# Kernel tuning notes

Hardware: AMD Instinct MI355X
Metric: run time of the kernel (lower is better)

The kernel has to match this reference:

```python
import jax, jax.numpy as jnp
import numpy as np

SX, SY, C, K = 256, 256, 3, 15
DD, DT, SIGMA = 5, 0.2, 0.65
C0 = tuple(i % C for i in range(K))
C1 = tuple(tuple(i for i in range(K) if i % C == c) for c in range(C))
MA = DD - SIGMA  # flow magnitude bound


def _sobel(A):
    # A: (X, Y, c) -> (X, Y, 2, c); matches jsp.signal.convolve2d(..., mode='same')
    kx = jnp.array([[1., 0., -1.], [2., 0., -2.], [1., 0., -1.]], dtype=A.dtype)
    ky = kx.T
    # convolve2d flips the kernel; emulate true convolution by correlating with rot180 kernels
    kern = jnp.stack([jnp.rot90(ky, 2), jnp.rot90(kx, 2)])[:, None]  # (2,1,3,3): [grad_y, grad_x]
    x = jnp.transpose(A, (2, 0, 1))[:, None]                          # (c,1,X,Y)
    out = jax.lax.conv_general_dilated(x, kern, (1, 1), 'SAME')       # (c,2,X,Y)
    return jnp.transpose(out, (2, 3, 1, 0))                           # (X,Y,2,c)


def _reintegration(A, P, F):
    # Reintegration tracking, has_hidden=True, border='wall', mix='softmax'
    xs, ys = jnp.meshgrid(jnp.arange(SX), jnp.arange(SY))
    pos = (jnp.dstack((ys, xs)) + .5).astype(A.dtype)     # (X,Y,2) cell centers (row, col)
    mus = pos[..., None] + jnp.clip(DT * F, -MA, MA)      # (X,Y,2,C) target centers
    mus = jnp.clip(mus, SIGMA, SX - SIGMA)                # wall border
    shifts = jnp.array([(dx, dy) for dx in range(-DD, DD + 1) for dy in range(-DD, DD + 1)])
    cap = min(1., 2 * SIGMA)

    def step(sft):
        sh = (sft[0], sft[1])
        Ar = jnp.roll(A, sh, axis=(0, 1))
        Pr = jnp.roll(P, sh, axis=(0, 1))
        mur = jnp.roll(mus, sh, axis=(0, 1))
        dpmu = jnp.abs(pos[..., None] - mur)              # (X,Y,2,C)
        sz = .5 - dpmu + SIGMA
        area = jnp.prod(jnp.clip(sz, 0., cap), axis=2) / (4 * SIGMA ** 2)  # (X,Y,C)
        return Ar * area, Pr

    nA, nP = jax.vmap(step)(shifts)                       # (N,X,Y,C), (N,X,Y,K)
    expnA = jnp.exp(nA.sum(-1, keepdims=True)) - 1.       # softmax mix rule
    newA = nA.sum(0)
    newP = (nP * expnA).sum(0) / (expnA.sum(0) + 1e-10)
    return newA, newP


def _forward(A, P, fK_real, fK_imag, m, s):
    fK = fK_real + 1j * fK_imag                           # (X,Y,K) kernel FFTs
    fA = jnp.fft.fft2(A, axes=(0, 1))                     # (X,Y,C)
    fAk = jnp.take(fA, jnp.array(C0), axis=2)             # (X,Y,K) per-kernel source channel
    U = jnp.real(jnp.fft.ifft2(fK * fAk, axes=(0, 1)))    # (X,Y,K)
    U = (2. * jnp.exp(-((U - m) ** 2) / (2. * s ** 2)) - 1.) * P  # growth(U,m,s)*P
    U = jnp.dstack([U[:, :, C1[c]].sum(-1) for c in range(C)])    # (X,Y,C)
    F = _sobel(U)                                         # (X,Y,2,C)
    Cg = _sobel(A.sum(-1, keepdims=True))                 # (X,Y,2,1)
    alpha = jnp.clip((A[:, :, None, :] / 2.) ** 2, 0., 1.)
    F = jnp.clip(F * (1. - alpha) - Cg * alpha, -MA, MA)
    return _reintegration(A, P, F)


def setup_inputs() -> dict:
    key = jax.random.key(0)
    kA, kP, kr, km, ks, ka, kb, kw = jax.random.split(key, 8)
    A = jax.random.uniform(kA, (SX, SY, C), dtype=jnp.float32)
    P = jax.random.uniform(kP, (SX, SY, K), dtype=jnp.float32)
    R = 15.0
    r = jax.random.uniform(kr, (K,), minval=.2, maxval=1.)
    m = jax.random.uniform(km, (K,), minval=.05, maxval=.5, dtype=jnp.float32)
    s = jax.random.uniform(ks, (K,), minval=.001, maxval=.18, dtype=jnp.float32)
    a = jax.random.uniform(ka, (K, 3))
    b = jax.random.uniform(kb, (K, 3), minval=.001, maxval=1.)
    w = jax.random.uniform(kw, (K, 3), minval=.01, maxval=.5)
    mid = SX // 2
    D = jnp.linalg.norm(jnp.mgrid[-mid:mid, -mid:mid], axis=0)[..., None] / ((R + 15.) * r)  # (X,Y,K)
    Kk = jax.nn.sigmoid(-(D - 1.) * 10.) * (b * jnp.exp(-((D[..., None] - a) / w) ** 2)).sum(-1)
    nK = Kk / Kk.sum((0, 1), keepdims=True)
    fK = jnp.fft.fft2(jnp.fft.fftshift(nK, axes=(0, 1)), axes=(0, 1))
    return {"A": A, "P": P,
            "fK_real": jnp.real(fK).astype(jnp.float32),
            "fK_imag": jnp.imag(fK).astype(jnp.float32),
            "m": m, "s": s}


def reference(A, P, fK_real, fK_imag, m, s):
    return _forward(A, P, fK_real, fK_imag, m, s)
```

## Files before the change

### kernel.cpp

```cpp
#include <hip/hip_runtime.h>


#define XY  65536
#define NC  3
#define NK  15
#define WPAD 260

__device__ __forceinline__ float2 cmul(float2 a, float2 b) {
  return make_float2(a.x * b.x - a.y * b.y, a.x * b.y + a.y * b.x);
}

__device__ __forceinline__ void fft256_lds(float2* b0, float2* b1, int t, float sign) {
  float2* src = b0;
  float2* dst = b1;
#pragma unroll
  for (int stage = 0; stage < 4; ++stage) {
    __syncthreads();
    const int Ns = 1 << (2 * stage);
    float2 v0 = src[t];
    float2 v1 = src[t + 64];
    float2 v2 = src[t + 128];
    float2 v3 = src[t + 192];
    const int jm = t & (Ns - 1);
    float ang = sign * 6.283185307179586f * (float)jm / (float)(Ns * 4);
    float sn, cs;
    __sincosf(ang, &sn, &cs);
    float2 w1 = make_float2(cs, sn);
    float2 w2 = cmul(w1, w1);
    float2 w3 = cmul(w2, w1);
    v1 = cmul(v1, w1);
    v2 = cmul(v2, w2);
    v3 = cmul(v3, w3);
    float2 a0 = make_float2(v0.x + v2.x, v0.y + v2.y);
    float2 a1 = make_float2(v0.x - v2.x, v0.y - v2.y);
    float2 a2 = make_float2(v1.x + v3.x, v1.y + v3.y);
    float2 a3 = make_float2(v1.x - v3.x, v1.y - v3.y);
    float2 ia3 = make_float2(-sign * a3.y, sign * a3.x);
    const int idxD = ((t >> (2 * stage)) << (2 * stage)) * 4 + jm;
    dst[idxD]          = make_float2(a0.x + a2.x, a0.y + a2.y);
    dst[idxD + Ns]     = make_float2(a1.x + ia3.x, a1.y + ia3.y);
    dst[idxD + 2 * Ns] = make_float2(a0.x - a2.x, a0.y - a2.y);
    dst[idxD + 3 * Ns] = make_float2(a1.x - ia3.x, a1.y - ia3.y);
    float2* tmp = src; src = dst; dst = tmp;
  }
  __syncthreads();
}

__global__ __launch_bounds__(256) void k_prep(const float* __restrict__ A,
                                              const float* __restrict__ P,
                                              float* __restrict__ Aplan,
                                              float* __restrict__ Asum,
                                              float* __restrict__ Pplan) {
  const int b = blockIdx.x * 256 + threadIdx.x;
  float a0 = A[b * 3 + 0], a1 = A[b * 3 + 1], a2 = A[b * 3 + 2];
  Aplan[0 * XY + b] = a0;
  Aplan[1 * XY + b] = a1;
  Aplan[2 * XY + b] = a2;
  Asum[b] = a0 + a1 + a2;
#pragma unroll
  for (int k = 0; k < NK; ++k) Pplan[k * XY + b] = P[b * NK + k];
}

__global__ __launch_bounds__(256) void k_rowfft(const float* __restrict__ Aplan,
                                                float2* __restrict__ RF) {
  __shared__ float2 lds0[4 * WPAD], lds1[4 * WPAD];
  const int tid = threadIdx.x;
  const int w = tid >> 6, lane = tid & 63;
  const int c = blockIdx.x >> 6;
  const int x = ((blockIdx.x & 63) << 2) + w;
  float2* b0 = lds0 + w * WPAD;
  float2* b1 = lds1 + w * WPAD;
  const float* src = Aplan + c * XY + x * 256;
#pragma unroll
  for (int r = 0; r < 4; ++r) {
    int y = lane + 64 * r;
    b0[y] = make_float2(src[y], 0.0f);
  }
  fft256_lds(b0, b1, lane, -1.0f);
#pragma unroll
  for (int r = 0; r < 4; ++r) {
    int y = lane + 64 * r;
    RF[(c * 256 + x) * 256 + y] = b0[y];
  }
}

__global__ __launch_bounds__(512, 1) void k_colfft(const float* __restrict__ fKr,
                                                   const float* __restrict__ fKi,
                                                   const float2* __restrict__ RF,
                                                   float2* __restrict__ T2) {
  __shared__ float2 lds0[8 * WPAD];
  __shared__ float2 lds1[8 * WPAD];
  const int tid = threadIdx.x;
  const int k = blockIdx.x >> 5;
  const int y0 = (blockIdx.x & 31) << 3;
  const int c = k % 3;

  {
    const int q = tid & 3;
#pragma unroll
    for (int r = 0; r < 2; ++r) {
      const int x = (tid >> 2) + (r << 7);
      const float4* src = (const float4*)(RF + (c * XY + x * 256 + y0));
      float4 v = src[q];
      lds0[(2 * q) * WPAD + x]     = make_float2(v.x, v.y);
      lds0[(2 * q + 1) * WPAD + x] = make_float2(v.z, v.w);
    }
  }

  const int w = tid >> 6, lane = tid & 63;
  float2* b0 = lds0 + w * WPAD;
  float2* b1 = lds1 + w * WPAD;
  fft256_lds(b0, b1, lane, -1.0f);

  const int y = y0 + w;
  float2 fa[4];
#pragma unroll
  for (int r = 0; r < 4; ++r) fa[r] = b0[lane + 64 * r];
#pragma unroll
  for (int r = 0; r < 4; ++r) {
    const int x = lane + 64 * r;
    const int fi = (x * 256 + y) * NK + k;
    float2 Kv = make_float2(fKr[fi], fKi[fi]);
    b0[x] = cmul(Kv, fa[r]);
  }
  fft256_lds(b0, b1, lane, 1.0f);

  {
    const int q = tid & 3;
#pragma unroll
    for (int r = 0; r < 2; ++r) {
      const int x = (tid >> 2) + (r << 7);
      float2 v0 = lds0[(2 * q) * WPAD + x];
      float2 v1 = lds0[(2 * q + 1) * WPAD + x];
      float4* dst = (float4*)(T2 + (k * XY + x * 256 + y0));
      dst[q] = make_float4(v0.x, v0.y, v1.x, v1.y);
    }
  }
}

__global__ __launch_bounds__(320, 1) void k_irowfft_growth(const float2* __restrict__ T2,
                                                           const float* __restrict__ Pplan,
                                                           const float* __restrict__ m,
                                                           const float* __restrict__ s,
                                                           float* __restrict__ Ucol) {
  __shared__ float2 lds0[5 * WPAD];
  __shared__ float2 lds1[5 * WPAD];
  __shared__ float accs[5 * WPAD];
  const int tid = threadIdx.x;
  const int x = blockIdx.x & 255;
  const int c = blockIdx.x >> 8;
  const int j = tid >> 6, lane = tid & 63;
  const int k = c + 3 * j;

  float2* b0 = lds0 + j * WPAD;
  float2* b1 = lds1 + j * WPAD;
  const float2* src = T2 + (k * XY + x * 256);
#pragma unroll
  for (int r = 0; r < 4; ++r) {
    int y = lane + 64 * r;
    b0[y] = src[y];
  }
  fft256_lds(b0, b1, lane, 1.0f);

  const float mk = m[k];
  const float sk = s[k];
  const float inv2s2 = 0.5f / (sk * sk);
  const float* pk = Pplan + k * XY + x * 256;
#pragma unroll
  for (int r = 0; r < 4; ++r) {
    int y = lane + 64 * r;
    float U = b0[y].x * (1.0f / 65536.0f);
    float d = U - mk;
    float g = 2.0f * __expf(-d * d * inv2s2) - 1.0f;
    accs[j * WPAD + y] = g * pk[y];
  }
  __syncthreads();
  if (tid < 256) {
    float sum = 0.f;
#pragma unroll
    for (int j2 = 0; j2 < 5; ++j2) sum += accs[j2 * WPAD + tid];
    Ucol[c * XY + x * 256 + tid] = sum;
  }
}

#define UROW 14
#define UCOLW 38
#define FROW 12
#define FCOLW 36
#define LPAD 40
__global__ __launch_bounds__(256, 2) void k_flow_reint(const float* __restrict__ Aplan,
                                                       const float* __restrict__ Asum,
                                                       const float* __restrict__ Ucol,
                                                       const float* __restrict__ Pplan,
                                                       float* __restrict__ outA,
                                                       float* __restrict__ outP) {
  __shared__ float smem[3 * UROW * LPAD + UROW * LPAD + 6 * FROW * LPAD + 3 * FROW * LPAD];
  float* Uc = smem;
  float* As = Uc + 3 * UROW * LPAD;
  float* Ft = As + UROW * LPAD;
  float* At = Ft + 6 * FROW * LPAD;
  float* PoutS = smem;
  float* AoutS = smem + 8 * 480;

  const int tid = threadIdx.x;
  const int x0 = (blockIdx.x >> 3) << 3;
  const int y0 = (blockIdx.x & 7) << 5;

  for (int i = tid; i < UROW * UCOLW; i += 256) {
    const int lx = i / UCOLW, ly = i - lx * UCOLW;
    const int gx = (x0 - 3 + lx) & 255;
    const int gy = (y0 - 3 + ly) & 255;
    const int g = gx * 256 + gy;
    Uc[0 * UROW * LPAD + lx * LPAD + ly] = Ucol[0 * XY + g];
    Uc[1 * UROW * LPAD + lx * LPAD + ly] = Ucol[1 * XY + g];
    Uc[2 * UROW * LPAD + lx * LPAD + ly] = Ucol[2 * XY + g];
    As[lx * LPAD + ly] = Asum[g];
  }
  __syncthreads();

  const float MA = 4.35f;
  for (int i = tid; i < FROW * FCOLW; i += 256) {
    const int j = i / FCOLW, l = i - j * FCOLW;
    const int wx = (x0 - 2 + j) & 255;
    const int wy = (y0 - 2 + l) & 255;
    const bool xm = (wx != 0), xp = (wx != 255);
    const bool ym = (wy != 0), yp = (wy != 255);
    float a00 = (xm && ym) ? As[(j) * LPAD + l] : 0.f;
    float a01 = xm ? As[(j) * LPAD + l + 1] : 0.f;
    float a02 = (xm && yp) ? As[(j) * LPAD + l + 2] : 0.f;
    float a10 = ym ? As[(j + 1) * LPAD + l] : 0.f;
    float a12 = yp ? As[(j + 1) * LPAD + l + 2] : 0.f;
    float a20 = (xp && ym) ? As[(j + 2) * LPAD + l] : 0.f;
    float a21 = xp ? As[(j + 2) * LPAD + l + 1] : 0.f;
    float a22 = (xp && yp) ? As[(j + 2) * LPAD + l + 2] : 0.f;
    float cg0 = (a20 + 2.f * a21 + a22) - (a00 + 2.f * a01 + a02);
    float cg1 = (a02 + 2.f * a12 + a22) - (a00 + 2.f * a10 + a20);
    const int wb = wx * 256 + wy;
#pragma unroll
    for (int c = 0; c < NC; ++c) {
      const float* up = Uc + c * UROW * LPAD;
      float u00 = (xm && ym) ? up[(j) * LPAD + l] : 0.f;
      float u01 = xm ? up[(j) * LPAD + l + 1] : 0.f;
      float u02 = (xm && yp) ? up[(j) * LPAD + l + 2] : 0.f;
      float u10 = ym ? up[(j + 1) * LPAD + l] : 0.f;
      float u12 = yp ? up[(j + 1) * LPAD + l + 2] : 0.f;
      float u20 = (xp && ym) ? up[(j + 2) * LPAD + l] : 0.f;
      float u21 = xp ? up[(j + 2) * LPAD + l + 1] : 0.f;
      float u22 = (xp && yp) ? up[(j + 2) * LPAD + l + 2] : 0.f;
      float f0 = (u20 + 2.f * u21 + u22) - (u00 + 2.f * u01 + u02);
      float f1 = (u02 + 2.f * u12 + u22) - (u00 + 2.f * u10 + u20);
      float av = Aplan[c * XY + wb];
      float ah = av * 0.5f;
      float al = fminf(ah * ah, 1.0f);
      f0 = fminf(fmaxf(f0 * (1.f - al) - cg0 * al, -MA), MA);
      f1 = fminf(fmaxf(f1 * (1.f - al) - cg1 * al, -MA), MA);
      Ft[(0 * 3 + c) * FROW * LPAD + j * LPAD + l] = f0;
      Ft[(1 * 3 + c) * FROW * LPAD + j * LPAD + l] = f1;
      At[c * FROW * LPAD + j * LPAD + l] = av;
    }
  }
  __syncthreads();

  const int tr = tid >> 5, tcol = tid & 31;
  const int tx = x0 + tr, ty = y0 + tcol;
  const float SIGMA = 0.65f;
  const float INV4S2 = 1.0f / (4.0f * 0.65f * 0.65f);
  const float DT = 0.2f;
  const float px = tx + 0.5f;
  const float py = ty + 0.5f;

  float accA[3] = {0.f, 0.f, 0.f};
  float accP[NK];
#pragma unroll
  for (int k = 0; k < NK; ++k) accP[k] = 0.f;
  float esum = 0.f;

  for (int dx = -2; dx <= 2; ++dx) {
    for (int dy = -2; dy <= 2; ++dy) {
      const int j = tr - dx + 2;
      const int l = tcol - dy + 2;
      const int sx = (tx - dx) & 255;
      const int sy = (ty - dy) & 255;
      const float spx = sx + 0.5f;
      const float spy = sy + 0.5f;
      float sumnA = 0.f;
      float nAc[3];
#pragma unroll
      for (int c = 0; c < NC; ++c) {
        float f0 = Ft[(0 * 3 + c) * FROW * LPAD + j * LPAD + l];
        float f1 = Ft[(1 * 3 + c) * FROW * LPAD + j * LPAD + l];
        float mu0 = fminf(fmaxf(spx + DT * f0, SIGMA), 256.f - SIGMA);
        float mu1 = fminf(fmaxf(spy + DT * f1, SIGMA), 256.f - SIGMA);
        float sz0 = 0.5f - fabsf(px - mu0) + SIGMA;
        float sz1 = 0.5f - fabsf(py - mu1) + SIGMA;
        sz0 = fminf(fmaxf(sz0, 0.f), 1.f);
        sz1 = fminf(fmaxf(sz1, 0.f), 1.f);
        float area = sz0 * sz1 * INV4S2;
        float na = At[c * FROW * LPAD + j * LPAD + l] * area;
        nAc[c] = na;
        sumnA += na;
      }
      if (__any(sumnA != 0.f)) {
        float e = __expf(sumnA) - 1.0f;
        accA[0] += nAc[0];
        accA[1] += nAc[1];
        accA[2] += nAc[2];
        esum += e;
        const int sb = sx * 256 + sy;
#pragma unroll
        for (int k = 0; k < NK; ++k) accP[k] += Pplan[k * XY + sb] * e;
      }
    }
  }
  const float inv = 1.0f / (esum + 1e-10f);

  __syncthreads();
#pragma unroll
  for (int c = 0; c < NC; ++c) AoutS[tr * 96 + tcol * 3 + c] = accA[c];
#pragma unroll
  for (int k = 0; k < NK; ++k) PoutS[tr * 480 + tcol * 15 + k] = accP[k] * inv;
  __syncthreads();
  for (int i = tid; i < 8 * 96; i += 256) {
    const int row = i / 96, off = i - row * 96;
    outA[((x0 + row) * 256 + y0) * 3 + off] = AoutS[i];
  }
  for (int i = tid; i < 8 * 480; i += 256) {
    const int row = i / 480, off = i - row * 480;
    outP[((x0 + row) * 256 + y0) * NK + off] = PoutS[i];
  }
}

extern "C" void kernel_launch(void* const* d_in, const int* in_sizes, int n_in,
                              void* d_out, int out_size, void* d_ws, size_t ws_size,
                              hipStream_t stream) {
  const float* A   = (const float*)d_in[0];
  const float* P   = (const float*)d_in[1];
  const float* fKr = (const float*)d_in[2];
  const float* fKi = (const float*)d_in[3];
  const float* m   = (const float*)d_in[4];
  const float* s   = (const float*)d_in[5];

  float* ws = (float*)d_ws;
  float2* RF    = (float2*)ws;
  float2* T2    = RF + NC * XY;
  float*  Ucol  = (float*)(T2 + NK * XY);
  float*  Aplan = Ucol + NC * XY;
  float*  Asum  = Aplan + NC * XY;
  float*  Pplan = Asum + XY;

  float* outA = (float*)d_out;
  float* outP = outA + NC * XY;

  k_prep<<<256, 256, 0, stream>>>(A, P, Aplan, Asum, Pplan);
  k_rowfft<<<NC * 64, 256, 0, stream>>>(Aplan, RF);
  k_colfft<<<NK * 32, 512, 0, stream>>>(fKr, fKi, RF, T2);
  k_irowfft_growth<<<NC * 256, 320, 0, stream>>>(T2, Pplan, m, s, Ucol);
  k_flow_reint<<<256, 256, 0, stream>>>(Aplan, Asum, Ucol, Pplan, outA, outP);
}
```

Measured before the change: 114.6 us.

## Fuse all stages into one cooperative persistent kernel with grid syncs

Replaces the five kernel launches with one cooperative kernel of 512 blocks that separates the stages (row FFT plus prep, column FFT with kernel multiply, inverse row FFT with growth, flow and reintegration) with grid.sync. The row FFT now reads A directly instead of waiting for the planar copy and runs alongside prep. Column FFT blocks shrink to 4 columns each. The five-way growth reduction is moved out of the inverse-FFT stage: per-kernel growth values go to a larger G buffer that the final stage sums when building its tile. This removes launch gaps, but adds grid barrier cost, extra traffic for G, and leaves half the blocks idle in the last stage.

```diff
diff --git a/kernel.cpp b/kernel.cpp
--- a/kernel.cpp
+++ b/kernel.cpp
@@ -1,4 +1,7 @@
 #include <hip/hip_runtime.h>
+#include <hip/hip_cooperative_groups.h>
+
+namespace cg = cooperative_groups;
 
 
 #define XY  65536
@@ -46,287 +49,257 @@
   __syncthreads();
 }
 
-__global__ __launch_bounds__(256) void k_prep(const float* __restrict__ A,
-                                              const float* __restrict__ P,
-                                              float* __restrict__ Aplan,
-                                              float* __restrict__ Asum,
-                                              float* __restrict__ Pplan) {
-  const int b = blockIdx.x * 256 + threadIdx.x;
-  float a0 = A[b * 3 + 0], a1 = A[b * 3 + 1], a2 = A[b * 3 + 2];
-  Aplan[0 * XY + b] = a0;
-  Aplan[1 * XY + b] = a1;
-  Aplan[2 * XY + b] = a2;
-  Asum[b] = a0 + a1 + a2;
-#pragma unroll
-  for (int k = 0; k < NK; ++k) Pplan[k * XY + b] = P[b * NK + k];
-}
-
-__global__ __launch_bounds__(256) void k_rowfft(const float* __restrict__ Aplan,
-                                                float2* __restrict__ RF) {
-  __shared__ float2 lds0[4 * WPAD], lds1[4 * WPAD];
-  const int tid = threadIdx.x;
-  const int w = tid >> 6, lane = tid & 63;
-  const int c = blockIdx.x >> 6;
-  const int x = ((blockIdx.x & 63) << 2) + w;
-  float2* b0 = lds0 + w * WPAD;
-  float2* b1 = lds1 + w * WPAD;
-  const float* src = Aplan + c * XY + x * 256;
-#pragma unroll
-  for (int r = 0; r < 4; ++r) {
-    int y = lane + 64 * r;
-    b0[y] = make_float2(src[y], 0.0f);
-  }
-  fft256_lds(b0, b1, lane, -1.0f);
-#pragma unroll
-  for (int r = 0; r < 4; ++r) {
-    int y = lane + 64 * r;
-    RF[(c * 256 + x) * 256 + y] = b0[y];
-  }
-}
-
-__global__ __launch_bounds__(512, 1) void k_colfft(const float* __restrict__ fKr,
-                                                   const float* __restrict__ fKi,
-                                                   const float2* __restrict__ RF,
-                                                   float2* __restrict__ T2) {
-  __shared__ float2 lds0[8 * WPAD];
-  __shared__ float2 lds1[8 * WPAD];
-  const int tid = threadIdx.x;
-  const int k = blockIdx.x >> 5;
-  const int y0 = (blockIdx.x & 31) << 3;
-  const int c = k % 3;
-
-  {
-    const int q = tid & 3;
-#pragma unroll
-    for (int r = 0; r < 2; ++r) {
-      const int x = (tid >> 2) + (r << 7);
-      const float4* src = (const float4*)(RF + (c * XY + x * 256 + y0));
-      float4 v = src[q];
-      lds0[(2 * q) * WPAD + x]     = make_float2(v.x, v.y);
-      lds0[(2 * q + 1) * WPAD + x] = make_float2(v.z, v.w);
-    }
-  }
-
-  const int w = tid >> 6, lane = tid & 63;
-  float2* b0 = lds0 + w * WPAD;
-  float2* b1 = lds1 + w * WPAD;
-  fft256_lds(b0, b1, lane, -1.0f);
-
-  const int y = y0 + w;
-  float2 fa[4];
-#pragma unroll
-  for (int r = 0; r < 4; ++r) fa[r] = b0[lane + 64 * r];
-#pragma unroll
-  for (int r = 0; r < 4; ++r) {
-    const int x = lane + 64 * r;
-    const int fi = (x * 256 + y) * NK + k;
-    float2 Kv = make_float2(fKr[fi], fKi[fi]);
-    b0[x] = cmul(Kv, fa[r]);
-  }
-  fft256_lds(b0, b1, lane, 1.0f);
-
-  {
-    const int q = tid & 3;
-#pragma unroll
-    for (int r = 0; r < 2; ++r) {
-      const int x = (tid >> 2) + (r << 7);
-      float2 v0 = lds0[(2 * q) * WPAD + x];
-      float2 v1 = lds0[(2 * q + 1) * WPAD + x];
-      float4* dst = (float4*)(T2 + (k * XY + x * 256 + y0));
-      dst[q] = make_float4(v0.x, v0.y, v1.x, v1.y);
-    }
-  }
-}
-
-__global__ __launch_bounds__(320, 1) void k_irowfft_growth(const float2* __restrict__ T2,
-                                                           const float* __restrict__ Pplan,
-                                                           const float* __restrict__ m,
-                                                           const float* __restrict__ s,
-                                                           float* __restrict__ Ucol) {
-  __shared__ float2 lds0[5 * WPAD];
-  __shared__ float2 lds1[5 * WPAD];
-  __shared__ float accs[5 * WPAD];
-  const int tid = threadIdx.x;
-  const int x = blockIdx.x & 255;
-  const int c = blockIdx.x >> 8;
-  const int j = tid >> 6, lane = tid & 63;
-  const int k = c + 3 * j;
-
-  float2* b0 = lds0 + j * WPAD;
-  float2* b1 = lds1 + j * WPAD;
-  const float2* src = T2 + (k * XY + x * 256);
-#pragma unroll
-  for (int r = 0; r < 4; ++r) {
-    int y = lane + 64 * r;
-    b0[y] = src[y];
-  }
-  fft256_lds(b0, b1, lane, 1.0f);
-
-  const float mk = m[k];
-  const float sk = s[k];
-  const float inv2s2 = 0.5f / (sk * sk);
-  const float* pk = Pplan + k * XY + x * 256;
-#pragma unroll
-  for (int r = 0; r < 4; ++r) {
-    int y = lane + 64 * r;
-    float U = b0[y].x * (1.0f / 65536.0f);
-    float d = U - mk;
-    float g = 2.0f * __expf(-d * d * inv2s2) - 1.0f;
-    accs[j * WPAD + y] = g * pk[y];
-  }
-  __syncthreads();
-  if (tid < 256) {
-    float sum = 0.f;
-#pragma unroll
-    for (int j2 = 0; j2 < 5; ++j2) sum += accs[j2 * WPAD + tid];
-    Ucol[c * XY + x * 256 + tid] = sum;
-  }
-}
-
 #define UROW 14
 #define UCOLW 38
 #define FROW 12
 #define FCOLW 36
 #define LPAD 40
-__global__ __launch_bounds__(256, 2) void k_flow_reint(const float* __restrict__ Aplan,
-                                                       const float* __restrict__ Asum,
-                                                       const float* __restrict__ Ucol,
-                                                       const float* __restrict__ Pplan,
-                                                       float* __restrict__ outA,
-                                                       float* __restrict__ outP) {
-  __shared__ float smem[3 * UROW * LPAD + UROW * LPAD + 6 * FROW * LPAD + 3 * FROW * LPAD];
-  float* Uc = smem;
-  float* As = Uc + 3 * UROW * LPAD;
-  float* Ft = As + UROW * LPAD;
-  float* At = Ft + 6 * FROW * LPAD;
-  float* PoutS = smem;
-  float* AoutS = smem + 8 * 480;
-
+
+__global__ __launch_bounds__(256, 2) void k_fused(
+    const float* __restrict__ A, const float* __restrict__ P,
+    const float* __restrict__ fKr, const float* __restrict__ fKi,
+    const float* __restrict__ m, const float* __restrict__ s,
+    float2* __restrict__ RF, float2* __restrict__ T2,
+    float* __restrict__ G, float* __restrict__ Aplan,
+    float* __restrict__ Asum, float* __restrict__ Pplan,
+    float* __restrict__ outA, float* __restrict__ outP) {
+  cg::grid_group grid = cg::this_grid();
+  __shared__ float2 smem2[3280];
+  float2* fbuf = smem2;
+  float* smem = (float*)smem2;
   const int tid = threadIdx.x;
-  const int x0 = (blockIdx.x >> 3) << 3;
-  const int y0 = (blockIdx.x & 7) << 5;
-
-  for (int i = tid; i < UROW * UCOLW; i += 256) {
-    const int lx = i / UCOLW, ly = i - lx * UCOLW;
-    const int gx = (x0 - 3 + lx) & 255;
-    const int gy = (y0 - 3 + ly) & 255;
-    const int g = gx * 256 + gy;
-    Uc[0 * UROW * LPAD + lx * LPAD + ly] = Ucol[0 * XY + g];
-    Uc[1 * UROW * LPAD + lx * LPAD + ly] = Ucol[1 * XY + g];
-    Uc[2 * UROW * LPAD + lx * LPAD + ly] = Ucol[2 * XY + g];
-    As[lx * LPAD + ly] = Asum[g];
-  }
-  __syncthreads();
-
-  const float MA = 4.35f;
-  for (int i = tid; i < FROW * FCOLW; i += 256) {
-    const int j = i / FCOLW, l = i - j * FCOLW;
-    const int wx = (x0 - 2 + j) & 255;
-    const int wy = (y0 - 2 + l) & 255;
-    const bool xm = (wx != 0), xp = (wx != 255);
-    const bool ym = (wy != 0), yp = (wy != 255);
-    float a00 = (xm && ym) ? As[(j) * LPAD + l] : 0.f;
-    float a01 = xm ? As[(j) * LPAD + l + 1] : 0.f;
-    float a02 = (xm && yp) ? As[(j) * LPAD + l + 2] : 0.f;
-    float a10 = ym ? As[(j + 1) * LPAD + l] : 0.f;
-    float a12 = yp ? As[(j + 1) * LPAD + l + 2] : 0.f;
-    float a20 = (xp && ym) ? As[(j + 2) * LPAD + l] : 0.f;
-    float a21 = xp ? As[(j + 2) * LPAD + l + 1] : 0.f;
-    float a22 = (xp && yp) ? As[(j + 2) * LPAD + l + 2] : 0.f;
-    float cg0 = (a20 + 2.f * a21 + a22) - (a00 + 2.f * a01 + a02);
-    float cg1 = (a02 + 2.f * a12 + a22) - (a00 + 2.f * a10 + a20);
-    const int wb = wx * 256 + wy;
-#pragma unroll
-    for (int c = 0; c < NC; ++c) {
-      const float* up = Uc + c * UROW * LPAD;
-      float u00 = (xm && ym) ? up[(j) * LPAD + l] : 0.f;
-      float u01 = xm ? up[(j) * LPAD + l + 1] : 0.f;
-      float u02 = (xm && yp) ? up[(j) * LPAD + l + 2] : 0.f;
-      float u10 = ym ? up[(j + 1) * LPAD + l] : 0.f;
-      float u12 = yp ? up[(j + 1) * LPAD + l + 2] : 0.f;
-      float u20 = (xp && ym) ? up[(j + 2) * LPAD + l] : 0.f;
-      float u21 = xp ? up[(j + 2) * LPAD + l + 1] : 0.f;
-      float u22 = (xp && yp) ? up[(j + 2) * LPAD + l + 2] : 0.f;
-      float f0 = (u20 + 2.f * u21 + u22) - (u00 + 2.f * u01 + u02);
-      float f1 = (u02 + 2.f * u12 + u22) - (u00 + 2.f * u10 + u20);
-      float av = Aplan[c * XY + wb];
-      float ah = av * 0.5f;
-      float al = fminf(ah * ah, 1.0f);
-      f0 = fminf(fmaxf(f0 * (1.f - al) - cg0 * al, -MA), MA);
-      f1 = fminf(fmaxf(f1 * (1.f - al) - cg1 * al, -MA), MA);
-      Ft[(0 * 3 + c) * FROW * LPAD + j * LPAD + l] = f0;
-      Ft[(1 * 3 + c) * FROW * LPAD + j * LPAD + l] = f1;
-      At[c * FROW * LPAD + j * LPAD + l] = av;
-    }
-  }
-  __syncthreads();
-
-  const int tr = tid >> 5, tcol = tid & 31;
-  const int tx = x0 + tr, ty = y0 + tcol;
-  const float SIGMA = 0.65f;
-  const float INV4S2 = 1.0f / (4.0f * 0.65f * 0.65f);
-  const float DT = 0.2f;
-  const float px = tx + 0.5f;
-  const float py = ty + 0.5f;
-
-  float accA[3] = {0.f, 0.f, 0.f};
-  float accP[NK];
-#pragma unroll
-  for (int k = 0; k < NK; ++k) accP[k] = 0.f;
-  float esum = 0.f;
-
-  for (int dx = -2; dx <= 2; ++dx) {
-    for (int dy = -2; dy <= 2; ++dy) {
-      const int j = tr - dx + 2;
-      const int l = tcol - dy + 2;
-      const int sx = (tx - dx) & 255;
-      const int sy = (ty - dy) & 255;
-      const float spx = sx + 0.5f;
-      const float spy = sy + 0.5f;
-      float sumnA = 0.f;
-      float nAc[3];
+  const int bid = blockIdx.x;
+  const int w = tid >> 6, lane = tid & 63;
+
+  if (bid < 192) {
+    const int g = bid * 4 + w;
+    const int c = g >> 8, x = g & 255;
+    float2* b0 = fbuf + w * WPAD;
+    float2* b1 = fbuf + (4 + w) * WPAD;
+#pragma unroll
+    for (int r = 0; r < 4; ++r) {
+      int y = lane + 64 * r;
+      b0[y] = make_float2(A[(x * 256 + y) * NC + c], 0.0f);
+    }
+    fft256_lds(b0, b1, lane, -1.0f);
+#pragma unroll
+    for (int r = 0; r < 4; ++r) {
+      int y = lane + 64 * r;
+      RF[(c * 256 + x) * 256 + y] = b0[y];
+    }
+  } else if (bid < 448) {
+    const int b = (bid - 192) * 256 + tid;
+    float a0 = A[b * 3 + 0], a1 = A[b * 3 + 1], a2 = A[b * 3 + 2];
+    Aplan[0 * XY + b] = a0;
+    Aplan[1 * XY + b] = a1;
+    Aplan[2 * XY + b] = a2;
+    Asum[b] = a0 + a1 + a2;
+#pragma unroll
+    for (int k = 0; k < NK; ++k) Pplan[k * XY + b] = P[b * NK + k];
+  }
+  grid.sync();
+
+  for (int tb = bid; tb < 960; tb += 512) {
+    const int k = tb >> 6;
+    const int y0 = (tb & 63) << 2;
+    const int c = k % 3;
+#pragma unroll
+    for (int r = 0; r < 2; ++r) {
+      const float4* srcp = (const float4*)(RF + (c * XY + tid * 256 + y0));
+      float4 v = srcp[r];
+      fbuf[(2 * r) * WPAD + tid]     = make_float2(v.x, v.y);
+      fbuf[(2 * r + 1) * WPAD + tid] = make_float2(v.z, v.w);
+    }
+    float2* b0 = fbuf + w * WPAD;
+    float2* b1 = fbuf + (4 + w) * WPAD;
+    fft256_lds(b0, b1, lane, -1.0f);
+    const int y = y0 + w;
+    float2 fa[4];
+#pragma unroll
+    for (int r = 0; r < 4; ++r) fa[r] = b0[lane + 64 * r];
+#pragma unroll
+    for (int r = 0; r < 4; ++r) {
+      const int x = lane + 64 * r;
+      const int fi = (x * 256 + y) * NK + k;
+      float2 Kv = make_float2(fKr[fi], fKi[fi]);
+      b0[x] = cmul(Kv, fa[r]);
+    }
+    fft256_lds(b0, b1, lane, 1.0f);
+#pragma unroll
+    for (int r = 0; r < 2; ++r) {
+      float2 v0 = fbuf[(2 * r) * WPAD + tid];
+      float2 v1 = fbuf[(2 * r + 1) * WPAD + tid];
+      ((float4*)(T2 + (k * XY + tid * 256 + y0)))[r] =
+          make_float4(v0.x, v0.y, v1.x, v1.y);
+    }
+    __syncthreads();
+  }
+  grid.sync();
+
+  for (int tb = bid; tb < 960; tb += 512) {
+    const int g = tb * 4 + w;
+    const int k = g >> 8, x = g & 255;
+    float2* b0 = fbuf + w * WPAD;
+    float2* b1 = fbuf + (4 + w) * WPAD;
+    const float2* srcp = T2 + (k * XY + x * 256);
+#pragma unroll
+    for (int r = 0; r < 4; ++r) {
+      int y = lane + 64 * r;
+      b0[y] = srcp[y];
+    }
+    fft256_lds(b0, b1, lane, 1.0f);
+    const float mk = m[k];
+    const float sk = s[k];
+    const float inv2s2 = 0.5f / (sk * sk);
+    const float* pk = Pplan + k * XY + x * 256;
+    float* gk = G + k * XY + x * 256;
+#pragma unroll
+    for (int r = 0; r < 4; ++r) {
+      int y = lane + 64 * r;
+      float U = b0[y].x * (1.0f / 65536.0f);
+      float d = U - mk;
+      float gr = 2.0f * __expf(-d * d * inv2s2) - 1.0f;
+      gk[y] = gr * pk[y];
+    }
+    __syncthreads();
+  }
+  grid.sync();
+
+  if (bid < 256) {
+    float* Uc = smem;
+    float* As = Uc + 3 * UROW * LPAD;
+    float* Ft = As + UROW * LPAD;
+    float* At = Ft + 6 * FROW * LPAD;
+    float* PoutS = smem;
+    float* AoutS = smem + 8 * 480;
+
+    const int x0 = (bid >> 3) << 3;
+    const int y0 = (bid & 7) << 5;
+
+    for (int i = tid; i < UROW * UCOLW; i += 256) {
+      const int lx = i / UCOLW, ly = i - lx * UCOLW;
+      const int gx = (x0 - 3 + lx) & 255;
+      const int gy = (y0 - 3 + ly) & 255;
+      const int gb = gx * 256 + gy;
+      As[lx * LPAD + ly] = Asum[gb];
 #pragma unroll
       for (int c = 0; c < NC; ++c) {
-        float f0 = Ft[(0 * 3 + c) * FROW * LPAD + j * LPAD + l];
-        float f1 = Ft[(1 * 3 + c) * FROW * LPAD + j * LPAD + l];
-        float mu0 = fminf(fmaxf(spx + DT * f0, SIGMA), 256.f - SIGMA);
-        float mu1 = fminf(fmaxf(spy + DT * f1, SIGMA), 256.f - SIGMA);
-        float sz0 = 0.5f - fabsf(px - mu0) + SIGMA;
-        float sz1 = 0.5f - fabsf(py - mu1) + SIGMA;
-        sz0 = fminf(fmaxf(sz0, 0.f), 1.f);
-        sz1 = fminf(fmaxf(sz1, 0.f), 1.f);
-        float area = sz0 * sz1 * INV4S2;
-        float na = At[c * FROW * LPAD + j * LPAD + l] * area;
-        nAc[c] = na;
-        sumnA += na;
+        float su = 0.f;
+#pragma unroll
+        for (int j = 0; j < 5; ++j) su += G[(c + 3 * j) * XY + gb];
+        Uc[c * UROW * LPAD + lx * LPAD + ly] = su;
       }
-      if (__any(sumnA != 0.f)) {
-        float e = __expf(sumnA) - 1.0f;
-        accA[0] += nAc[0];
-        accA[1] += nAc[1];
-        accA[2] += nAc[2];
-        esum += e;
-        const int sb = sx * 256 + sy;
-#pragma unroll
-        for (int k = 0; k < NK; ++k) accP[k] += Pplan[k * XY + sb] * e;
+    }
+    __syncthreads();
+
+    const float MA = 4.35f;
+    for (int i = tid; i < FROW * FCOLW; i += 256) {
+      const int j = i / FCOLW, l = i - j * FCOLW;
+      const int wx = (x0 - 2 + j) & 255;
+      const int wy = (y0 - 2 + l) & 255;
+      const bool xm = (wx != 0), xp = (wx != 255);
+      const bool ym = (wy != 0), yp = (wy != 255);
+      float a00 = (xm && ym) ? As[(j) * LPAD + l] : 0.f;
+      float a01 = xm ? As[(j) * LPAD + l + 1] : 0.f;
+      float a02 = (xm && yp) ? As[(j) * LPAD + l + 2] : 0.f;
+      float a10 = ym ? As[(j + 1) * LPAD + l] : 0.f;
+      float a12 = yp ? As[(j + 1) * LPAD + l + 2] : 0.f;
+      float a20 = (xp && ym) ? As[(j + 2) * LPAD + l] : 0.f;
+      float a21 = xp ? As[(j + 2) * LPAD + l + 1] : 0.f;
+      float a22 = (xp && yp) ? As[(j + 2) * LPAD + l + 2] : 0.f;
+      float cg0 = (a20 + 2.f * a21 + a22) - (a00 + 2.f * a01 + a02);
+      float cg1 = (a02 + 2.f * a12 + a22) - (a00 + 2.f * a10 + a20);
+      const int wb = wx * 256 + wy;
+#pragma unroll
+      for (int c = 0; c < NC; ++c) {
+        const float* up = Uc + c * UROW * LPAD;
+        float u00 = (xm && ym) ? up[(j) * LPAD + l] : 0.f;
+        float u01 = xm ? up[(j) * LPAD + l + 1] : 0.f;
+        float u02 = (xm && yp) ? up[(j) * LPAD + l + 2] : 0.f;
+        float u10 = ym ? up[(j + 1) * LPAD + l] : 0.f;
+        float u12 = yp ? up[(j + 1) * LPAD + l + 2] : 0.f;
+        float u20 = (xp && ym) ? up[(j + 2) * LPAD + l] : 0.f;
+        float u21 = xp ? up[(j + 2) * LPAD + l + 1] : 0.f;
+        float u22 = (xp && yp) ? up[(j + 2) * LPAD + l + 2] : 0.f;
+        float f0 = (u20 + 2.f * u21 + u22) - (u00 + 2.f * u01 + u02);
+        float f1 = (u02 + 2.f * u12 + u22) - (u00 + 2.f * u10 + u20);
+        float av = Aplan[c * XY + wb];
+        float ah = av * 0.5f;
+        float al = fminf(ah * ah, 1.0f);
+        f0 = fminf(fmaxf(f0 * (1.f - al) - cg0 * al, -MA), MA);
+        f1 = fminf(fmaxf(f1 * (1.f - al) - cg1 * al, -MA), MA);
+        Ft[(0 * 3 + c) * FROW * LPAD + j * LPAD + l] = f0;
+        Ft[(1 * 3 + c) * FROW * LPAD + j * LPAD + l] = f1;
+        At[c * FROW * LPAD + j * LPAD + l] = av;
       }
     }
-  }
-  const float inv = 1.0f / (esum + 1e-10f);
-
-  __syncthreads();
-#pragma unroll
-  for (int c = 0; c < NC; ++c) AoutS[tr * 96 + tcol * 3 + c] = accA[c];
-#pragma unroll
-  for (int k = 0; k < NK; ++k) PoutS[tr * 480 + tcol * 15 + k] = accP[k] * inv;
-  __syncthreads();
-  for (int i = tid; i < 8 * 96; i += 256) {
-    const int row = i / 96, off = i - row * 96;
-    outA[((x0 + row) * 256 + y0) * 3 + off] = AoutS[i];
-  }
-  for (int i = tid; i < 8 * 480; i += 256) {
-    const int row = i / 480, off = i - row * 480;
-    outP[((x0 + row) * 256 + y0) * NK + off] = PoutS[i];
+    __syncthreads();
+
+    const int tr = tid >> 5, tcol = tid & 31;
+    const int tx = x0 + tr, ty = y0 + tcol;
+    const float SIGMA = 0.65f;
+    const float INV4S2 = 1.0f / (4.0f * 0.65f * 0.65f);
+    const float DT = 0.2f;
+    const float px = tx + 0.5f;
+    const float py = ty + 0.5f;
+    float accA[3] = {0.f, 0.f, 0.f};
+    float accP[NK];
+#pragma unroll
+    for (int k = 0; k < NK; ++k) accP[k] = 0.f;
+    float esum = 0.f;
+    for (int dx = -2; dx <= 2; ++dx) {
+      for (int dy = -2; dy <= 2; ++dy) {
+        const int j = tr - dx + 2;
+        const int l = tcol - dy + 2;
+        const int sx = (tx - dx) & 255;
+        const int sy = (ty - dy) & 255;
+        const float spx = sx + 0.5f;
+        const float spy = sy + 0.5f;
+        float sumnA = 0.f;
+        float nAc[3];
+#pragma unroll
+        for (int c = 0; c < NC; ++c) {
+          float f0 = Ft[(0 * 3 + c) * FROW * LPAD + j * LPAD + l];
+          float f1 = Ft[(1 * 3 + c) * FROW * LPAD + j * LPAD + l];
+          float mu0 = fminf(fmaxf(spx + DT * f0, SIGMA), 256.f - SIGMA);
+          float mu1 = fminf(fmaxf(spy + DT * f1, SIGMA), 256.f - SIGMA);
+          float sz0 = 0.5f - fabsf(px - mu0) + SIGMA;
+          float sz1 = 0.5f - fabsf(py - mu1) + SIGMA;
+          sz0 = fminf(fmaxf(sz0, 0.f), 1.f);
+          sz1 = fminf(fmaxf(sz1, 0.f), 1.f);
+          float area = sz0 * sz1 * INV4S2;
+          float na = At[c * FROW * LPAD + j * LPAD + l] * area;
+          nAc[c] = na;
+          sumnA += na;
+        }
+        if (__any(sumnA != 0.f)) {
+          float e = __expf(sumnA) - 1.0f;
+          accA[0] += nAc[0];
+          accA[1] += nAc[1];
+          accA[2] += nAc[2];
+          esum += e;
+          const int sb = sx * 256 + sy;
+#pragma unroll
+          for (int k = 0; k < NK; ++k) accP[k] += Pplan[k * XY + sb] * e;
+        }
+      }
+    }
+    const float inv = 1.0f / (esum + 1e-10f);
+
+    __syncthreads();
+#pragma unroll
+    for (int c = 0; c < NC; ++c) AoutS[tr * 96 + tcol * 3 + c] = accA[c];
+#pragma unroll
+    for (int k = 0; k < NK; ++k) PoutS[tr * 480 + tcol * 15 + k] = accP[k] * inv;
+    __syncthreads();
+    for (int i = tid; i < 8 * 96; i += 256) {
+      const int row = i / 96, off = i - row * 96;
+      outA[((x0 + row) * 256 + y0) * 3 + off] = AoutS[i];
+    }
+    for (int i = tid; i < 8 * 480; i += 256) {
+      const int row = i / 480, off = i - row * 480;
+      outP[((x0 + row) * 256 + y0) * NK + off] = PoutS[i];
+    }
   }
 }
 
@@ -343,17 +316,18 @@
   float* ws = (float*)d_ws;
   float2* RF    = (float2*)ws;
   float2* T2    = RF + NC * XY;
-  float*  Ucol  = (float*)(T2 + NK * XY);
-  float*  Aplan = Ucol + NC * XY;
+  float*  G     = (float*)(T2 + NK * XY);
+  float*  Aplan = G + NK * XY;
   float*  Asum  = Aplan + NC * XY;
   float*  Pplan = Asum + XY;
 
   float* outA = (float*)d_out;
   float* outP = outA + NC * XY;
 
-  k_prep<<<256, 256, 0, stream>>>(A, P, Aplan, Asum, Pplan);
-  k_rowfft<<<NC * 64, 256, 0, stream>>>(Aplan, RF);
-  k_colfft<<<NK * 32, 512, 0, stream>>>(fKr, fKi, RF, T2);
-  k_irowfft_growth<<<NC * 256, 320, 0, stream>>>(T2, Pplan, m, s, Ucol);
-  k_flow_reint<<<256, 256, 0, stream>>>(Aplan, Asum, Ucol, Pplan, outA, outP);
+  void* args[] = {(void*)&A, (void*)&P, (void*)&fKr, (void*)&fKi,
+                  (void*)&m, (void*)&s, (void*)&RF, (void*)&T2,
+                  (void*)&G, (void*)&Aplan, (void*)&Asum, (void*)&Pplan,
+                  (void*)&outA, (void*)&outP};
+  hipLaunchCooperativeKernel((void*)k_fused, dim3(512), dim3(256), args, 0,
+                             stream);
 }
```

New measurement: 326.8 us. 2.85x slower.
